# Kernel tuning notes

Hardware: AMD Instinct MI355X
Metric: run time of the kernel (lower is better)

The kernel has to match this reference:

```python
import jax, jax.numpy as jnp
import numpy as np

EPS_D = 1e-12  # clamp for sqrt of pairwise distances (diag is exactly 0)


def tr2dist_small(Y):
    # Y: (B, k, N) -> (B, N, N); standard protein-folding coords->distance map
    k = Y.shape[1]
    Z = Y - jnp.mean(Y, axis=2, keepdims=True)
    n2 = jnp.sum(Z * Z, axis=1)                        # (B, N)
    D = n2[:, None, :] + n2[:, :, None] - 2.0 * jnp.einsum('bkn,bkm->bnm', Z, Z)
    D = 3.0 * D / k
    return jnp.sqrt(jnp.maximum(D, EPS_D))


def mean_masked(X, mask, axis, keepdims=True):
    return jnp.sum(X * mask, axis=axis, keepdims=keepdims) / jnp.sum(mask, axis=axis, keepdims=keepdims)


def get_graph_lap(X, mask):
    # X: (B, C, N), mask: (B, 1, N)
    B, C, N = X.shape
    mm = jnp.einsum('bin,bim->bnm', mask, mask)        # (B, N, N) pair mask
    X = X - mean_masked(X, mask, axis=2) * mask
    X = X / jnp.sqrt(jnp.sum(X * X, axis=2, keepdims=True) / jnp.sum(mask, axis=2, keepdims=True) + 1e-4)
    pos = 0.5 * jnp.linspace(0.0, 1.0, N)[None, :] * mask   # (B, 1, N)
    Xa = jnp.concatenate((X, pos), axis=1)
    Wd = tr2dist_small(Xa) * mm
    sigma = mean_masked(Wd, mm, axis=(1, 2))           # (B, 1, 1)
    Wd = jnp.exp(-Wd / sigma * 10.0) * mm
    Wsum = jnp.sum(Wd, axis=1)                         # (B, N)
    L = jnp.zeros_like(Wd) + Wsum[:, :, None] * jnp.eye(N, dtype=Wd.dtype)[None] - Wd
    L = 0.5 * (L + jnp.swapaxes(L, 1, 2))
    return L, Wd


def _forward(Z, mask, K0, Knet, W, Wend):
    h = 0.01
    m = mask[:, None, :]                               # (B, 1, N)
    Z = jnp.tanh(jnp.einsum('oc,bcn->bon', K0, Z)) * m
    nlayers = W.shape[0]
    for i in range(nlayers):
        L, _ = get_graph_lap(Z, m)
        Ki = Knet[i]
        Wi = W[i, :, :, :, 0]                          # (3, C, C) size-1 kernels
        cv = lambda w, x: jnp.einsum('oc,bcn->bon', w, x) * m     # conv1d, k=1
        cvT = lambda w, x: jnp.einsum('co,bcn->bon', w, x) * m    # conv_transpose1d, k=1
        mm1 = lambda x: jnp.einsum('bcn,bnm->bcm', x, L)
        Ai = Ki[0] * cv(Wi[0], Z) + mm1(Ki[1] * cv(Wi[1], Z)) + mm1(mm1(Ki[2] * cv(Wi[2], Z)))
        Ai = (Ai - mean_masked(Ai, m, axis=2)) * m
        Ai = Ai / jnp.sqrt(jnp.sum(Ai * Ai, axis=1, keepdims=True) + 0.001)
        Ai = jax.nn.relu(Ai)
        Ai = Ki[0] * cvT(Wi[0], Ai) + mm1(Ki[1] * cvT(Wi[1], Ai)) + mm1(mm1(Ki[2] * cvT(Wi[2], Ai)))
        Z = Z - h * Ai
    Zout = jnp.einsum('oc,bcn->bon', Wend[:, :, 0], Z) * m       # (B, chan_out, N)
    dists = tuple(tr2dist_small(Zout[:, 3 * i:3 * i + 3, :]) for i in range(Zout.shape[1] // 3))
    return dists + (Zout,)


def setup_inputs() -> dict:
    key = jax.random.key(0)
    ks = jax.random.split(key, 6)
    B, chan_in, chan_out, channels, N, nlayers = 16, 40, 3, 256, 1024, 6
    stdv0 = 0.1 * channels / chan_in
    return {
        'Z': jax.random.normal(ks[0], (B, chan_in, N), dtype=jnp.float32),
        'mask': jnp.ones((B, N), dtype=jnp.float32),
        'K0': jax.random.uniform(ks[1], (channels, chan_in), minval=-stdv0, maxval=stdv0, dtype=jnp.float32),
        'Knet': jax.random.uniform(ks[2], (nlayers, chan_out), minval=-stdv0, maxval=stdv0, dtype=jnp.float32),
        'W': jax.random.uniform(ks[3], (nlayers, 3, channels, channels, 1), minval=-0.1, maxval=0.1, dtype=jnp.float32),
        'Wend': 1e-4 * jax.random.normal(ks[4], (chan_out, channels, 1), dtype=jnp.float32),
    }


def reference(Z, mask, K0, Knet, W, Wend):
    return _forward(Z, mask, K0, Knet, W, Wend)
```

## Files before the change

kernel.cpp:

```cpp
#include <hip/hip_runtime.h>
#include <hip/hip_fp16.h>
#include <math.h>

#define BB 16
#define CIN 40
#define CH 256
#define NN 1024
#define NLAYERS 6

typedef unsigned short ush;
typedef __attribute__((ext_vector_type(8))) short bh8;
typedef __attribute__((ext_vector_type(8))) _Float16 h8;
typedef __attribute__((ext_vector_type(4))) float f4;

__device__ __forceinline__ ush bf16_rne(float x) {
  unsigned int u = __float_as_uint(x);
  u += 0x7fffu + ((u >> 16) & 1u);
  return (ush)(u >> 16);
}
__device__ __forceinline__ float bf16_f(ush h) {
  return __uint_as_float(((unsigned int)h) << 16);
}
__device__ __forceinline__ ush f2h(float x) {
  __half h = __float2half(x);
  return *(ush*)&h;
}
__device__ __forceinline__ float h2f(ush u) {
  __half h = *(__half*)&u;
  return __half2float(h);
}

#define GLD16(gp, lp) __builtin_amdgcn_global_load_lds( \
    (const __attribute__((address_space(1))) void*)(gp), \
    (__attribute__((address_space(3))) void*)(lp), 16, 0, 0)

__device__ __forceinline__ float blockReduceSum(float v) {
  __shared__ float sred[4];
  const int lane = threadIdx.x & 63;
  const int wid  = threadIdx.x >> 6;
  #pragma unroll
  for (int off = 32; off > 0; off >>= 1) v += __shfl_down(v, off, 64);
  __syncthreads();
  if (lane == 0) sred[wid] = v;
  __syncthreads();
  return sred[0] + sred[1] + sred[2] + sred[3];
}

__device__ __forceinline__ void stageA(
    const ush* __restrict__ Ah, const ush* __restrict__ Al, const int sA,
    const ush* __restrict__ Bh, const ush* __restrict__ Bl, const int sB,
    const int kt, ush* buf) {
  const int lane = threadIdx.x & 63;
  const int wid = threadIdx.x >> 6;
  const int srow = lane >> 2;
  const int sl = (lane & 3) ^ ((srow >> 1) & 3);
  #pragma unroll
  for (int cc = 0; cc < 8; cc++) {
    const int c = wid * 8 + cc;
    const ush* src;
    if (c < 8)       src = Ah + (size_t)(c * 16 + srow) * sA + kt + sl * 8;
    else if (c < 16) src = Al + (size_t)((c - 8) * 16 + srow) * sA + kt + sl * 8;
    else if (c < 24) src = Bh + (size_t)((c - 16) * 16 + srow) * sB + kt + sl * 8;
    else             src = Bl + (size_t)((c - 24) * 16 + srow) * sB + kt + sl * 8;
    GLD16(src, buf + c * 512 + lane * 8);
  }
}

__device__ __forceinline__ void computeA(const ush* buf, f4 acc[4][4]) {
  const int lane = threadIdx.x & 63;
  const int wid = threadIdx.x >> 6;
  const int wr = wid >> 1, wc = wid & 1;
  const int frow = lane & 15;
  const int slot8 = (((lane >> 4) ^ ((frow >> 1) & 3)) << 3);
  bh8 ah[4], al[4], bh_[4], bl_[4];
  #pragma unroll
  for (int mi = 0; mi < 4; mi++) {
    const int off = (wr * 64 + mi * 16 + frow) * 32 + slot8;
    ah[mi] = *(const bh8*)&buf[off];
    al[mi] = *(const bh8*)&buf[4096 + off];
  }
  #pragma unroll
  for (int ni = 0; ni < 4; ni++) {
    const int off = (wc * 64 + ni * 16 + frow) * 32 + slot8;
    bh_[ni] = *(const bh8*)&buf[8192 + off];
    bl_[ni] = *(const bh8*)&buf[12288 + off];
  }
  #pragma unroll
  for (int mi = 0; mi < 4; mi++)
    #pragma unroll
    for (int ni = 0; ni < 4; ni++) {
      acc[mi][ni] = __builtin_amdgcn_mfma_f32_16x16x32_bf16(ah[mi], bh_[ni], acc[mi][ni], 0, 0, 0);
      acc[mi][ni] = __builtin_amdgcn_mfma_f32_16x16x32_bf16(ah[mi], bl_[ni], acc[mi][ni], 0, 0, 0);
      acc[mi][ni] = __builtin_amdgcn_mfma_f32_16x16x32_bf16(al[mi], bh_[ni], acc[mi][ni], 0, 0, 0);
    }
}

__device__ __forceinline__ void stageCV(
    const ush* __restrict__ Ap, const int sA,
    const ush* __restrict__ Bh, const ush* __restrict__ Bl, const int sB,
    const int kt, ush* buf) {
  const int lane = threadIdx.x & 63;
  const int wid = threadIdx.x >> 6;
  const int srow = lane >> 2;
  const int sl = (lane & 3) ^ ((srow >> 1) & 3);
  #pragma unroll
  for (int cc = 0; cc < 6; cc++) {
    const int c = wid * 6 + cc;
    const ush* src;
    if (c < 8)       src = Ap + (size_t)(c * 16 + srow) * sA + kt + sl * 8;
    else if (c < 16) src = Bh + (size_t)((c - 8) * 16 + srow) * sB + kt + sl * 8;
    else             src = Bl + (size_t)((c - 16) * 16 + srow) * sB + kt + sl * 8;
    GLD16(src, buf + c * 512 + lane * 8);
// ... 4 lines not shown
  const int lane = threadIdx.x & 63;
  const int wid = threadIdx.x >> 6;
  const int wr = wid >> 1, wc = wid & 1;
  const int frow = lane & 15;
  const int slot8 = (((lane >> 4) ^ ((frow >> 1) & 3)) << 3);
  h8 a_[4], bh_[4], bl_[4];
  #pragma unroll
  for (int mi = 0; mi < 4; mi++) {
    const int off = (wr * 64 + mi * 16 + frow) * 32 + slot8;
    a_[mi] = *(const h8*)&buf[off];
  }
  #pragma unroll
  for (int ni = 0; ni < 4; ni++) {
    const int off = (wc * 64 + ni * 16 + frow) * 32 + slot8;
    bh_[ni] = *(const h8*)&buf[4096 + off];
    bl_[ni] = *(const h8*)&buf[8192 + off];
  }
  #pragma unroll
  for (int mi = 0; mi < 4; mi++)
    #pragma unroll
    for (int ni = 0; ni < 4; ni++) {
      acc[mi][ni] = __builtin_amdgcn_mfma_f32_16x16x32_f16(a_[mi], bh_[ni], acc[mi][ni], 0, 0, 0);
      acc[mi][ni] = __builtin_amdgcn_mfma_f32_16x16x32_f16(a_[mi], bl_[ni], acc[mi][ni], 0, 0, 0);
    }
}

__device__ __forceinline__ void stageMM(
    const ush* __restrict__ Ah, const ush* __restrict__ Al, const int sA,
    const ush* __restrict__ Bp, const int sB, const int kt, ush* buf) {
  const int lane = threadIdx.x & 63;
  const int wid = threadIdx.x >> 6;
  const int srow = lane >> 2;
  const int sl = (lane & 3) ^ ((srow >> 1) & 3);
  #pragma unroll
  for (int cc = 0; cc < 4; cc++) {
    const int c = wid * 4 + cc;
    const ush* src;
    if (c < 4)       src = Ah + (size_t)(c * 16 + srow) * sA + kt + sl * 8;
    else if (c < 8)  src = Al + (size_t)((c - 4) * 16 + srow) * sA + kt + sl * 8;
    else             src = Bp + (size_t)((c - 8) * 16 + srow) * sB + kt + sl * 8;
    GLD16(src, buf + c * 512 + lane * 8);
  }
}

__device__ __forceinline__ void computeMM(const ush* buf, f4 acc[4][2]) {
  const int lane = threadIdx.x & 63;
  const int wid = threadIdx.x >> 6;
  const int frow = lane & 15;
  const int slot8 = (((lane >> 4) ^ ((frow >> 1) & 3)) << 3);
  h8 ah[4], al[4], b_[2];
  #pragma unroll
  for (int mi = 0; mi < 4; mi++) {
    const int off = (mi * 16 + frow) * 32 + slot8;
    ah[mi] = *(const h8*)&buf[off];
    al[mi] = *(const h8*)&buf[2048 + off];
  }
  #pragma unroll
  for (int ni = 0; ni < 2; ni++) {
    const int off = (wid * 32 + ni * 16 + frow) * 32 + slot8;
    b_[ni] = *(const h8*)&buf[4096 + off];
  }
  #pragma unroll
  for (int mi = 0; mi < 4; mi++)
    #pragma unroll
    for (int ni = 0; ni < 2; ni++) {
      acc[mi][ni] = __builtin_amdgcn_mfma_f32_16x16x32_f16(ah[mi], b_[ni], acc[mi][ni], 0, 0, 0);
      acc[mi][ni] = __builtin_amdgcn_mfma_f32_16x16x32_f16(al[mi], b_[ni], acc[mi][ni], 0, 0, 0);
    }
}

__global__ void k0_kernel(const float* __restrict__ Zin, const float* __restrict__ K0,
                          const float* __restrict__ mask, float* __restrict__ Zc,
                          float* __restrict__ statS1, float* __restrict__ statS2) {
  const int b = blockIdx.y;
  const int o = blockIdx.x;
  __shared__ float w[CIN];
  if (threadIdx.x < CIN) w[threadIdx.x] = K0[o * CIN + threadIdx.x];
  __syncthreads();
  float s1 = 0.f, s2 = 0.f;
  for (int n = threadIdx.x; n < NN; n += 256) {
    float acc = 0.f;
    #pragma unroll
    for (int c = 0; c < CIN; c++) acc += w[c] * Zin[((size_t)b * CIN + c) * NN + n];
    const float z = tanhf(acc) * mask[b * NN + n];
    Zc[((size_t)b * CH + o) * NN + n] = z;
    s1 += z; s2 += z * z;
  }
  s1 = blockReduceSum(s1);
  s2 = blockReduceSum(s2);
  if (threadIdx.x == 0) {
    const size_t base = ((size_t)b * CH + o) * 8;
    statS1[base] = s1; statS2[base] = s2;
    #pragma unroll
    for (int k = 1; k < 8; k++) { statS1[base + k] = 0.f; statS2[base + k] = 0.f; }
  }
}

__global__ void masksum_kernel(const float* __restrict__ mask, float* __restrict__ msum,
                               float* __restrict__ posv) {
  const int b = blockIdx.x;
  float v = 0.f, p = 0.f;
  for (int n = threadIdx.x; n < NN; n += 256) {
    const float m = mask[b * NN + n];
    v += m;
    p += 0.5f * ((float)n * (1.0f / (NN - 1))) * m;
  }
  v = blockReduceSum(v);
  p = blockReduceSum(p);
  const float pm = p * (1.0f / NN);
  if (threadIdx.x == 0) msum[b] = v;
  for (int n = threadIdx.x; n < NN; n += 256)
    posv[b * NN + n] = 0.5f * ((float)n * (1.0f / (NN - 1))) * mask[b * NN + n] - pm;
}

__global__ void wprep_kernel(const float* __restrict__ W, ush* __restrict__ Wm,
                             ush* __restrict__ Wt) {
  __shared__ float t[64][65];
  const int mat = blockIdx.y;
  const int ty = blockIdx.x >> 2, tx = blockIdx.x & 3;
  const float* src = W + (size_t)mat * CH * CH;
  const int tid = threadIdx.x;
  const int lr = tid >> 2;
  const int lc = (tid & 3) * 16;
  float v[16];
  #pragma unroll
  for (int j = 0; j < 16; j += 4)
    *(float4*)&v[j] = *(const float4*)&src[(size_t)(ty * 64 + lr) * CH + tx * 64 + lc + j];
  ush hv[16];
  #pragma unroll
  for (int j = 0; j < 16; j++) {
    hv[j] = f2h(v[j]);
    t[lr][lc + j] = v[j];
  }
  const size_t offm = (size_t)mat * CH * CH + (size_t)(ty * 64 + lr) * CH + tx * 64 + lc;
  #pragma unroll
  for (int j = 0; j < 16; j += 4)
    *(ushort4*)&Wm[offm + j] = *(ushort4*)&hv[j];
  __syncthreads();
  #pragma unroll
  for (int j = 0; j < 16; j++) hv[j] = f2h(t[lc + j][lr]);
  const size_t offt = (size_t)mat * CH * CH + (size_t)(tx * 64 + lr) * CH + ty * 64 + lc;
  #pragma unroll
  for (int j = 0; j < 16; j += 4)
    *(ushort4*)&Wt[offt + j] = *(ushort4*)&hv[j];
}

__global__ void rowstatZ_kernel(const float* __restrict__ statS1, const float* __restrict__ statS2,
                                const float* __restrict__ msum, float* __restrict__ muZ,
                                float* __restrict__ rsZ) {
  const int b = blockIdx.x;
  const int c = threadIdx.x;
  const size_t base = ((size_t)b * CH + c) * 8;
  float S1 = 0.f, S2 = 0.f;
  #pragma unroll
  for (int k = 0; k < 8; k++) { S1 += statS1[base + k]; S2 += statS2[base + k]; }
  const float M = msum[b];
  const float mu = S1 / M;
  const float q = fmaxf(S2 - mu * S1, 0.f);
  muZ[b * CH + c] = mu;
  rsZ[b * CH + c] = 1.0f / sqrtf(q / M + 1e-4f);
}

__global__ void rowstatU_kernel(const float* __restrict__ statS1, const float* __restrict__ msum,
                                float* __restrict__ rmean) {
  const int b = blockIdx.x;
  const int c = threadIdx.x;
  const size_t base = ((size_t)b * CH + c) * 8;
  float S1 = 0.f;
  #pragma unroll
  for (int k = 0; k < 8; k++) S1 += statS1[base + k];
  rmean[b * CH + c] = S1 / msum[b];
}

__global__ void tsplitZ_kernel(const float* __restrict__ in, ush* __restrict__ Th,
                               ush* __restrict__ Tl) {
  __shared__ float t[32][65];
  const int b = blockIdx.z;
  const int n0 = blockIdx.x * 64;
  const int k0 = blockIdx.y * 32;
  const float* src = in + (size_t)b * CH * NN;
  const int tid = threadIdx.x;
  const int lr = tid >> 3;
  const int lc = (tid & 7) * 8;
  const int gk = k0 + lr;
  *(float4*)&t[lr][lc]     = *(const float4*)&src[(size_t)gk * NN + n0 + lc];
  *(float4*)&t[lr][lc + 4] = *(const float4*)&src[(size_t)gk * NN + n0 + lc + 4];
  __syncthreads();
  const int on = tid >> 2;
  const int ok = (tid & 3) * 8;
  ush hv[8], lv[8];
  #pragma unroll
  for (int j = 0; j < 8; j++) {
    const float v = t[ok + j][on];
    hv[j] = f2h(v); lv[j] = f2h(v - h2f(hv[j]));
  }
  const size_t off = ((size_t)b * NN + n0 + on) * CH + k0 + ok;
  *(ushort4*)&Th[off] = *(ushort4*)&hv[0];
  *(ushort4*)&Th[off + 4] = *(ushort4*)&hv[4];
  *(ushort4*)&Tl[off] = *(ushort4*)&lv[0];
  *(ushort4*)&Tl[off + 4] = *(ushort4*)&lv[4];
}

__global__ void tsplitY2_kernel(const ush* __restrict__ Zsh, const ush* __restrict__ Zsl,
                                const float* __restrict__ mask, const float* __restrict__ muZ,
                                const float* __restrict__ rsZ, ush* __restrict__ Th,
                                ush* __restrict__ Tl, float* __restrict__ n2part) {
  const int b = blockIdx.z;
  const int n0 = blockIdx.x * 64;
  const int k0 = blockIdx.y * 32;
  const int tid = threadIdx.x;
  const int n = n0 + (tid >> 2);
  const int kc = k0 + (tid & 3) * 8;
  const float mn = mask[b * NN + n];
  const size_t zoff = ((size_t)b * NN + n) * CH + kc;
  const ushort4 h0 = *(const ushort4*)&Zsh[zoff];
  const ushort4 h1 = *(const ushort4*)&Zsh[zoff + 4];
  const ushort4 l0 = *(const ushort4*)&Zsl[zoff];
  const ushort4 l1 = *(const ushort4*)&Zsl[zoff + 4];
  const float4 mu0 = *(const float4*)&muZ[b * CH + kc];
  const float4 mu1 = *(const float4*)&muZ[b * CH + kc + 4];
  const float4 rs0 = *(const float4*)&rsZ[b * CH + kc];
  const float4 rs1 = *(const float4*)&rsZ[b * CH + kc + 4];
  float val[8];
  val[0] = (h2f(h0.x) + h2f(l0.x) - mu0.x * mn) * rs0.x;
  val[1] = (h2f(h0.y) + h2f(l0.y) - mu0.y * mn) * rs0.y;
  val[2] = (h2f(h0.z) + h2f(l0.z) - mu0.z * mn) * rs0.z;
  val[3] = (h2f(h0.w) + h2f(l0.w) - mu0.w * mn) * rs0.w;
  val[4] = (h2f(h1.x) + h2f(l1.x) - mu1.x * mn) * rs1.x;
  val[5] = (h2f(h1.y) + h2f(l1.y) - mu1.y * mn) * rs1.y;
  val[6] = (h2f(h1.z) + h2f(l1.z) - mu1.z * mn) * rs1.z;
  val[7] = (h2f(h1.w) + h2f(l1.w) - mu1.w * mn) * rs1.w;
  float s = 0.f;
  ush hv[8], lv[8];
  #pragma unroll
  for (int j = 0; j < 8; j++) {
    s += val[j] * val[j];
    hv[j] = bf16_rne(val[j]);
    lv[j] = bf16_rne(val[j] - bf16_f(hv[j]));
  }
  const size_t off = ((size_t)b * NN + n) * CH + kc;
  *(ushort4*)&Th[off] = *(ushort4*)&hv[0];
  *(ushort4*)&Th[off + 4] = *(ushort4*)&hv[4];
  *(ushort4*)&Tl[off] = *(ushort4*)&lv[0];
  *(ushort4*)&Tl[off + 4] = *(ushort4*)&lv[4];
  s += __shfl_xor(s, 1, 64);
  s += __shfl_xor(s, 2, 64);
  if ((tid & 3) == 0) n2part[((size_t)b * 8 + blockIdx.y) * NN + n] = s;
}

__global__ void n2red_kernel(const float* __restrict__ n2part, const float* __restrict__ posv,
                             float* __restrict__ n2) {
  const int idx = blockIdx.x * 256 + threadIdx.x;
  const int b = idx >> 10;
  const float pv = posv[idx];
  float s = pv * pv;
  #pragma unroll
  for (int kb = 0; kb < 8; kb++) s += n2part[((size_t)b * 8 + kb) * NN + (idx & 1023)];
  n2[idx] = s;
}

__global__ __launch_bounds__(256, 2)
void gram_v5_kernel(const ush* __restrict__ Yth, const ush* __restrict__ Ytl,
                    const float* __restrict__ n2, const float* __restrict__ mask,
                    const float* __restrict__ posv, ush* __restrict__ Dp,
                    float* __restrict__ sigpart) {
  __shared__ ush lds[32768];
  const int bid = blockIdx.x;
  const int logical = (bid & 7) * 72 + (bid >> 3);
  const int b = logical / 36;
  int t = logical - b * 36;
  int ty = 0;
  while (t >= 8 - ty) { t -= 8 - ty; ++ty; }
  const int tx = ty + t;
  const int i0 = ty * 128;
  const int j0 = tx * 128;
  const ush* Ah = Yth + (size_t)b * NN * CH + (size_t)i0 * CH;
  const ush* Al = Ytl + (size_t)b * NN * CH + (size_t)i0 * CH;
  const ush* Bh = Yth + (size_t)b * NN * CH + (size_t)j0 * CH;
  const ush* Bl = Ytl + (size_t)b * NN * CH + (size_t)j0 * CH;
  f4 acc[4][4];
  const f4 z4 = {0.f, 0.f, 0.f, 0.f};
  #pragma unroll
  for (int mi = 0; mi < 4; mi++)
    #pragma unroll
    for (int ni = 0; ni < 4; ni++) acc[mi][ni] = z4;
  stageA(Ah, Al, CH, Bh, Bl, CH, 0, lds);
  __syncthreads();
  int pb = 0;
  for (int kt = 32; kt < CH; kt += 32) {
    stageA(Ah, Al, CH, Bh, Bl, CH, kt, lds + (pb ^ 1) * 16384);
    computeA(lds + pb * 16384, acc);
    __syncthreads();
    pb ^= 1;
  }
  computeA(lds + pb * 16384, acc);
  const int lane = threadIdx.x & 63;
  const int wid = threadIdx.x >> 6;
  const int wr = wid >> 1, wc = wid & 1;
  const int frow = lane & 15, hh = lane >> 4;
  const float scale = 3.0f / 257.0f;
  float lsum = 0.f;
  #pragma unroll
  for (int ni = 0; ni < 4; ni++) {
    const int jl = wc * 64 + ni * 16 + frow;
    const int j = j0 + jl;
    const float n2j = n2[b * NN + j];
    const float mkj = mask[b * NN + j];
    const float pj = posv[b * NN + j];
    #pragma unroll
    for (int mi = 0; mi < 4; mi++) {
      const int il = wr * 64 + mi * 16 + hh * 4;
      ush dv[4];
      #pragma unroll
      for (int r = 0; r < 4; r++) {
        const int i = i0 + il + r;
        const float g = acc[mi][ni][r] + posv[b * NN + i] * pj;
        const float D = scale * (n2[b * NN + i] + n2j - 2.0f * g);
        const float d = sqrtf(fmaxf(D, 1e-12f));
        const float mmv = mask[b * NN + i] * mkj;
        const float wd = d * mmv;
        lsum += wd * mmv;
        dv[r] = f2h(wd);
      }
      if (ty != tx) {
        uint2 mr;
        mr.x = (unsigned)dv[0] | ((unsigned)dv[1] << 16);
        mr.y = (unsigned)dv[2] | ((unsigned)dv[3] << 16);
        *(uint2*)&Dp[((size_t)b * NN + j) * NN + i0 + il] = mr;
      }
      #pragma unroll
      for (int r = 0; r < 4; r++) {
        const unsigned v = dv[r];
        const unsigned vp = (unsigned)__shfl_xor((int)v, 1, 64);
        if ((frow & 1) == 0)
          *(unsigned*)&Dp[((size_t)b * NN + i0 + il + r) * NN + j] = v | (vp << 16);
      }
    }
  }
  if (ty != tx) lsum *= 2.0f;
  #pragma unroll
  for (int off = 32; off > 0; off >>= 1) lsum += __shfl_down(lsum, off, 64);
  __syncthreads();
  float* rbuf = (float*)lds;
  if (lane == 0) rbuf[wid] = lsum;
  __syncthreads();
  if (threadIdx.x == 0)
    sigpart[(size_t)b * 64 + ty * 8 + tx] = rbuf[0] + rbuf[1] + rbuf[2] + rbuf[3];
}

__global__ void sigfinal_kernel(const float* __restrict__ sigpart, const float* __restrict__ msum,
                                float* __restrict__ fbuf) {
  const int b = blockIdx.x;
  float v = 0.f;
  if (threadIdx.x < 64) {
    const int ty = threadIdx.x >> 3, tx = threadIdx.x & 7;
    if (ty <= tx) v = sigpart[b * 64 + threadIdx.x];
  }
  v = blockReduceSum(v);
  if (threadIdx.x == 0) { const float ms = msum[b]; fbuf[b] = -10.0f * ms * ms / v; }
}

__global__ void expw3_kernel(const ush* __restrict__ Dp, const float* __restrict__ mask,
                             const float* __restrict__ fbuf, ush* __restrict__ Wp) {
  const int b = blockIdx.y, n = blockIdx.x;
  const float fb = fbuf[b];
  const float mn = mask[b * NN + n];
  const size_t roff = ((size_t)b * NN + n) * NN;
  const int t = threadIdx.x;
  const float4 mk = ((const float4*)(mask + b * NN))[t];
  const ushort4 dp = *(const ushort4*)&Dp[roff + t * 4];
  const float w0 = expf(fb * h2f(dp.x)) * mn * mk.x;
  const float w1 = expf(fb * h2f(dp.y)) * mn * mk.y;
  const float w2 = expf(fb * h2f(dp.z)) * mn * mk.z;
  const float w3 = expf(fb * h2f(dp.w)) * mn * mk.w;
  const float s = blockReduceSum(w0 + w1 + w2 + w3);
  float v0 = -w0, v1 = -w1, v2 = -w2, v3 = -w3;
  if ((n >> 2) == t) {
    const int r = n & 3;
    if (r == 0) v0 += s; else if (r == 1) v1 += s; else if (r == 2) v2 += s; else v3 += s;
  }
  ushort4 h4;
  h4.x = f2h(v0); h4.y = f2h(v1); h4.z = f2h(v2); h4.w = f2h(v3);
  *(ushort4*)&Wp[roff + t * 4] = h4;
}

__global__ __launch_bounds__(256, 3)
void cvall_kernel(const ush* __restrict__ Ap, const ush* __restrict__ Bth,
                  const ush* __restrict__ Btl, const float* __restrict__ mask,
                  const float* __restrict__ Kis, unsigned int* __restrict__ Cpack,
                  ush* __restrict__ C2h, ush* __restrict__ C2l) {
  __shared__ ush lds[24576];
  const int bid = blockIdx.x;
  const int logical = (bid & 7) * 96 + (bid >> 3);
  const int b = logical / 48;
  const int inner = logical - b * 48;
  const int c0g = inner & 7;
  const int r0g = inner >> 3;
  const int r0 = r0g * 128;
  const int c0 = c0g * 128;
  const ush* Aq = Ap + (size_t)r0 * CH;
  const ush* Bh = Bth + (size_t)b * NN * CH + (size_t)c0 * CH;
  const ush* Bl = Btl + (size_t)b * NN * CH + (size_t)c0 * CH;
  f4 acc[4][4];
  const f4 z4 = {0.f, 0.f, 0.f, 0.f};
  #pragma unroll
  for (int mi = 0; mi < 4; mi++)
    #pragma unroll
    for (int ni = 0; ni < 4; ni++) acc[mi][ni] = z4;
  stageCV(Aq, CH, Bh, Bl, CH, 0, lds);
  __syncthreads();
  int pb = 0;
  for (int kt = 32; kt < CH; kt += 32) {
    stageCV(Aq, CH, Bh, Bl, CH, kt, lds + (pb ^ 1) * 12288);
    computeCV(lds + pb * 12288, acc);
    __syncthreads();
    pb ^= 1;
  }
  computeCV(lds + pb * 12288, acc);
  const int lane = threadIdx.x & 63;
  const int wid = threadIdx.x >> 6;
  const int wr = wid >> 1, wc = wid & 1;
  const int frow = lane & 15, hh = lane >> 4;
  const float alpha = Kis[r0g >> 1];
  #pragma unroll
  for (int ni = 0; ni < 4; ni++) {
    const int jl = wc * 64 + ni * 16 + frow;
    const int col = c0 + jl;
    const float am = alpha * mask[b * NN + col];
    #pragma unroll
    for (int mi = 0; mi < 4; mi++) {
      const int il = wr * 64 + mi * 16 + hh * 4;
      #pragma unroll
      for (int r = 0; r < 4; r++) {
        const int row = r0 + il + r;
        const float v = acc[mi][ni][r] * am;
        const ush h = f2h(v);
        const ush l = f2h(v - h2f(h));
        const unsigned pv = (unsigned)h | ((unsigned)l << 16);
        const unsigned pvp = (unsigned)__shfl_xor((int)pv, 1, 64);
        if ((frow & 1) == 0) {
          if (r0g < 4) {
            uint2 w2; w2.x = pv; w2.y = pvp;
            *(uint2*)&Cpack[((size_t)b * 512 + row) * NN + col] = w2;
          } else {
            const size_t obase = ((size_t)b * 256 + (row - 512)) * NN + col;
            const unsigned hw = (pv & 0xffffu) | (pvp << 16);
            const unsigned lw = (pv >> 16) | (pvp & 0xffff0000u);
            *(unsigned*)&C2h[obase] = hw;
            *(unsigned*)&C2l[obase] = lw;
          }
        }
      }
    }
  }
}

template <int OUTMODE, int STATS>
// ... 75 lines not shown
  __syncthreads();
  if (OUTMODE == 0) {
    const int rrow = threadIdx.x >> 2;
    const int rch = (threadIdx.x & 3) * 32;
    const size_t obase = ((size_t)b * 256 + r0 + rrow) * NN + n0 + rch;
    #pragma unroll
    for (int g = 0; g < 4; g++) {
      unsigned int hw[4], lw[4];
      #pragma unroll
      for (int q = 0; q < 4; q++) {
        unsigned int h2[2], l2[2];
        #pragma unroll
        for (int e = 0; e < 2; e++) {
          const int jl = rch + g * 8 + q * 2 + e;
          const int slot = (rrow >> 2) ^ (jl & 15);
          const unsigned int v = tl[jl * 64 + slot * 4 + (rrow & 3)];
          h2[e] = v & 0xffffu; l2[e] = v >> 16;
        }
        hw[q] = h2[0] | (h2[1] << 16);
        lw[q] = l2[0] | (l2[1] << 16);
      }
      *(uint4*)&outH[obase + g * 8] = *(uint4*)hw;
      *(uint4*)&outL[obase + g * 8] = *(uint4*)lw;
    }
  } else {
    const int nloc = threadIdx.x >> 1;
    const int ch0 = (threadIdx.x & 1) * 32;
    #pragma unroll
    for (int half = 0; half < 2; half++) {
      unsigned int hw[8], lw[8];
      #pragma unroll
      for (int q = 0; q < 8; q++) {
        const int ila = ch0 + half * 16 + q * 2;
        const int ilb = ila + 1;
        const unsigned int va = tl[nloc * 64 + (((ila >> 2) ^ (nloc & 15)) << 2) + (ila & 3)];
        const unsigned int vb = tl[nloc * 64 + (((ilb >> 2) ^ (nloc & 15)) << 2) + (ilb & 3)];
        hw[q] = (va & 0xffffu) | (vb << 16);
        lw[q] = (va >> 16) | (vb & 0xffff0000u);
      }
      const size_t zoff = ((size_t)b * NN + n0 + nloc) * CH + r0 + ch0 + half * 16;
      *(uint4*)&outH[zoff] = *(uint4*)&hw[0];
      *(uint4*)&outH[zoff + 8] = *(uint4*)&hw[4];
      *(uint4*)&outL[zoff] = *(uint4*)&lw[0];
      *(uint4*)&outL[zoff + 8] = *(uint4*)&lw[4];
    }
  }
  if (STATS) {
    #pragma unroll
    for (int mi = 0; mi < 4; mi++)
      #pragma unroll
      for (int r = 0; r < 4; r++) {
        #pragma unroll
        for (int d = 1; d < 16; d <<= 1) {
          a1[mi][r] += __shfl_xor(a1[mi][r], d, 64);
          a2[mi][r] += __shfl_xor(a2[mi][r], d, 64);
        }
      }
    __syncthreads();
    float* s1b = (float*)lds;
    float* s2b = s1b + 256;
    if (frow == 0) {
      #pragma unroll
      for (int mi = 0; mi < 4; mi++)
        #pragma unroll
        for (int r = 0; r < 4; r++) {
          const int row = mi * 16 + hh * 4 + r;
          s1b[wid * 64 + row] = a1[mi][r];
          s2b[wid * 64 + row] = a2[mi][r];
        }
    }
    __syncthreads();
    if (threadIdx.x < 64) {
      const int row = threadIdx.x;
      const float p1 = s1b[row] + s1b[64 + row] + s1b[128 + row] + s1b[192 + row];
      const float p2 = s2b[row] + s2b[64 + row] + s2b[128 + row] + s2b[192 + row];
      const int nblk = n0 >> 7;
      statS1[((size_t)b * CH + r0 + row) * 8 + nblk] = p1;
      statS2[((size_t)b * CH + r0 + row) * 8 + nblk] = p2;
    }
  }
}

__global__ void csq_kernel(const ush* __restrict__ Uh, const ush* __restrict__ Ul,
                           const float* __restrict__ mask, const float* __restrict__ rmean,
                           float* __restrict__ part) {
  const int b = blockIdx.y, cc = blockIdx.x;
  const int n = threadIdx.x * 4;
  const float4 m4 = *(const float4*)&mask[b * NN + n];
  float4 s4 = {0.f, 0.f, 0.f, 0.f};
  for (int r = 0; r < 16; r++) {
    const int c = cc * 16 + r;
    const float rm = rmean[b * CH + c];
    const size_t uoff = ((size_t)b * 256 + c) * NN + n;
    const ushort4 uh = *(const ushort4*)&Uh[uoff];
    const ushort4 ul = *(const ushort4*)&Ul[uoff];
    float a;
    a = (h2f(uh.x) + h2f(ul.x) - rm) * m4.x; s4.x += a * a;
    a = (h2f(uh.y) + h2f(ul.y) - rm) * m4.y; s4.y += a * a;
    a = (h2f(uh.z) + h2f(ul.z) - rm) * m4.z; s4.z += a * a;
    a = (h2f(uh.w) + h2f(ul.w) - rm) * m4.w; s4.w += a * a;
  }
  *(float4*)&part[((size_t)(b * 16 + cc)) * NN + n] = s4;
}

__global__ void csq2_kernel(const float* __restrict__ part, float* __restrict__ rs) {
  const int b = blockIdx.y;
  const int n = blockIdx.x * 256 + threadIdx.x;
  float s = 0.001f;
  #pragma unroll
  for (int cc = 0; cc < 16; cc++) s += part[((size_t)(b * 16 + cc)) * NN + n];
  rs[b * NN + n] = 1.0f / sqrtf(s);
}

__global__ void tsplitN2_kernel(const ush* __restrict__ Uh, const ush* __restrict__ Ul,
                                const float* __restrict__ mask, const float* __restrict__ rmean,
                                const float* __restrict__ rs, ush* __restrict__ Th,
                                ush* __restrict__ Tl) {
  __shared__ float t[32][65];
  const int b = blockIdx.z;
  const int n0 = blockIdx.x * 64;
  const int k0 = blockIdx.y * 32;
  const int tid = threadIdx.x;
  const int lr = tid >> 3;
  const int lc = (tid & 7) * 8;
  const int gc = k0 + lr;
  const float rm = rmean[b * CH + gc];
  const float4 ma = *(const float4*)&mask[b * NN + n0 + lc];
  const float4 mb = *(const float4*)&mask[b * NN + n0 + lc + 4];
  const float4 ra = *(const float4*)&rs[b * NN + n0 + lc];
  const float4 rb = *(const float4*)&rs[b * NN + n0 + lc + 4];
  const size_t uoff = ((size_t)b * 256 + gc) * NN + n0 + lc;
  const ushort4 ha = *(const ushort4*)&Uh[uoff];
  const ushort4 hb = *(const ushort4*)&Uh[uoff + 4];
  const ushort4 la = *(const ushort4*)&Ul[uoff];
  const ushort4 lb = *(const ushort4*)&Ul[uoff + 4];
  t[lr][lc + 0] = fmaxf((h2f(ha.x) + h2f(la.x) - rm) * ma.x * ra.x, 0.f);
  t[lr][lc + 1] = fmaxf((h2f(ha.y) + h2f(la.y) - rm) * ma.y * ra.y, 0.f);
  t[lr][lc + 2] = fmaxf((h2f(ha.z) + h2f(la.z) - rm) * ma.z * ra.z, 0.f);
  t[lr][lc + 3] = fmaxf((h2f(ha.w) + h2f(la.w) - rm) * ma.w * ra.w, 0.f);
  t[lr][lc + 4] = fmaxf((h2f(hb.x) + h2f(lb.x) - rm) * mb.x * rb.x, 0.f);
  t[lr][lc + 5] = fmaxf((h2f(hb.y) + h2f(lb.y) - rm) * mb.y * rb.y, 0.f);
  t[lr][lc + 6] = fmaxf((h2f(hb.z) + h2f(lb.z) - rm) * mb.z * rb.z, 0.f);
  t[lr][lc + 7] = fmaxf((h2f(hb.w) + h2f(lb.w) - rm) * mb.w * rb.w, 0.f);
  __syncthreads();
  const int on = tid >> 2;
  const int ok = (tid & 3) * 8;
  ush hv[8], lv[8];
  #pragma unroll
  for (int j = 0; j < 8; j++) {
    const float v = t[ok + j][on];
    hv[j] = f2h(v); lv[j] = f2h(v - h2f(hv[j]));
  }
  const size_t off = ((size_t)b * NN + n0 + on) * CH + k0 + ok;
  *(ushort4*)&Th[off] = *(ushort4*)&hv[0];
  *(ushort4*)&Th[off + 4] = *(ushort4*)&hv[4];
  *(ushort4*)&Tl[off] = *(ushort4*)&lv[0];
  *(ushort4*)&Tl[off + 4] = *(ushort4*)&lv[4];
}

__global__ void zout_kernel(const float* __restrict__ Z, const float* __restrict__ Wend,
                            const float* __restrict__ mask, float* __restrict__ outZ,
                            float* __restrict__ Zcent) {
  const int b = blockIdx.x;
  __shared__ float w[3 * CH];
  for (int i = threadIdx.x; i < 3 * CH; i += 256) w[i] = Wend[i];
  __syncthreads();
  float a[3][4];
  #pragma unroll
  for (int j = 0; j < 4; j++) { a[0][j] = 0.f; a[1][j] = 0.f; a[2][j] = 0.f; }
  const float* Zb = Z + (size_t)b * CH * NN;
  for (int c = 0; c < CH; c++) {
    const float w0 = w[c], w1 = w[CH + c], w2 = w[2 * CH + c];
    #pragma unroll
    for (int j = 0; j < 4; j++) {
      float zv = Zb[(size_t)c * NN + threadIdx.x + j * 256];
      a[0][j] += w0 * zv; a[1][j] += w1 * zv; a[2][j] += w2 * zv;
    }
  }
  float sum[3] = {0.f, 0.f, 0.f};
  #pragma unroll
  for (int j = 0; j < 4; j++) {
    const int n = threadIdx.x + j * 256;
    const float mv = mask[b * NN + n];
    #pragma unroll
    for (int o = 0; o < 3; o++) {
      a[o][j] *= mv;
      outZ[((size_t)b * 3 + o) * NN + n] = a[o][j];
      sum[o] += a[o][j];
    }
  }
  for (int o = 0; o < 3; o++) {
    float s = blockReduceSum(sum[o]);
    const float mean = s * (1.0f / NN);
    #pragma unroll
    for (int j = 0; j < 4; j++) {
      const int n = threadIdx.x + j * 256;
      Zcent[((size_t)b * 3 + o) * NN + n] = a[o][j] - mean;
    }
  }
}

__global__ void dist_kernel(const float* __restrict__ Zcent, float* __restrict__ outD) {
  const int b = blockIdx.z;
  const int n = blockIdx.y;
  const int m = blockIdx.x * 256 + threadIdx.x;
  const float* Zb = Zcent + (size_t)b * 3 * NN;
  const float x0 = Zb[n], x1 = Zb[NN + n], x2 = Zb[2 * NN + n];
  const float d0 = x0 - Zb[m], d1 = x1 - Zb[NN + m], d2 = x2 - Zb[2 * NN + m];
  const float D = d0 * d0 + d1 * d1 + d2 * d2;
  outD[((size_t)b * NN + n) * NN + m] = sqrtf(fmaxf(D, 1e-12f));
}

extern "C" void kernel_launch(void* const* d_in, const int* in_sizes, int n_in,
                              void* d_out, int out_size, void* d_ws, size_t ws_size,
                              hipStream_t stream) {
  const float* Zin  = (const float*)d_in[0];
  const float* mask = (const float*)d_in[1];
  const float* K0   = (const float*)d_in[2];
  const float* Knet = (const float*)d_in[3];
  const float* W    = (const float*)d_in[4];
  const float* Wend = (const float*)d_in[5];
  float* out = (float*)d_out;

  ush* Wp = (ush*)out;
  ush* Dp = Wp + (size_t)BB * NN * NN;
  float* outZ = out + (size_t)BB * NN * NN;

  float* p = (float*)d_ws;
  float* uni = p; p += (size_t)BB * 768 * NN;
  ush* Yth = (ush*)uni;
  ush* Ytl = Yth + (size_t)BB * NN * CH;
  unsigned int* Cpack = (unsigned int*)uni;
  ush* C2h = (ush*)(uni + (size_t)BB * 512 * NN);
  ush* C2l = C2h + (size_t)BB * 256 * NN;

  float* Zcur = p; p += (size_t)BB * CH * NN;
  ush* Thb = (ush*)p; p += (size_t)BB * NN * CH / 2;
  ush* Tlb = (ush*)p; p += (size_t)BB * NN * CH / 2;
  ush* Zsh = (ush*)p; p += (size_t)BB * NN * CH / 2;
  ush* Zsl = (ush*)p; p += (size_t)BB * NN * CH / 2;
  ush* Wm = (ush*)p; p += (size_t)18 * CH * CH / 2;
  ush* Wt = (ush*)p; p += (size_t)18 * CH * CH / 2;
  float* n2b   = p; p += BB * NN;
  float* rsb   = p; p += BB * NN;
  float* msum  = p; p += BB;
  float* posv  = p; p += BB * NN;
  float* sigp  = p; p += BB * 64;
  float* fbuf  = p; p += BB;
  float* rmeanb= p; p += BB * CH;
  float* muZ   = p; p += BB * CH;
  float* rsZ   = p; p += BB * CH;
  float* statS1= p; p += (size_t)BB * CH * 8;
  float* statS2= p; p += (size_t)BB * CH * 8;
  float* n2part= p; p += (size_t)BB * 8 * NN;
  float* partb = p; p += (size_t)BB * 16 * NN;
  float* Zcent = p; p += BB * 3 * NN;

  const dim3 gtsZ(NN / 64, CH / 32, BB);
  const size_t sC = (size_t)512 * NN;
  const size_t sT = (size_t)CH * NN;

  masksum_kernel<<<BB, 256, 0, stream>>>(mask, msum, posv);
  wprep_kernel<<<dim3(16, 18), 256, 0, stream>>>(W, Wm, Wt);
  k0_kernel<<<dim3(CH, BB), 256, 0, stream>>>(Zin, K0, mask, Zcur, statS1, statS2);
  tsplitZ_kernel<<<gtsZ, 256, 0, stream>>>(Zcur, Zsh, Zsl);

  for (int layer = 0; layer < NLAYERS; layer++) {
    rowstatZ_kernel<<<BB, 256, 0, stream>>>(statS1, statS2, msum, muZ, rsZ);
    tsplitY2_kernel<<<gtsZ, 256, 0, stream>>>(Zsh, Zsl, mask, muZ, rsZ, Yth, Ytl, n2part);
    n2red_kernel<<<BB * NN / 256, 256, 0, stream>>>(n2part, posv, n2b);
    gram_v5_kernel<<<576, 256, 0, stream>>>(Yth, Ytl, n2b, mask, posv, Dp, sigp);
    sigfinal_kernel<<<BB, 256, 0, stream>>>(sigp, msum, fbuf);
    expw3_kernel<<<dim3(NN, BB), 256, 0, stream>>>(Dp, mask, fbuf, Wp);

    const ush* Am = Wm + (size_t)layer * 3 * CH * CH;
    const ush* At = Wt + (size_t)layer * 3 * CH * CH;
    const float* Ki = Knet + layer * 3;

    cvall_kernel<<<768, 256, 0, stream>>>(Am, Zsh, Zsl, mask, Ki, Cpack, C2h, C2l);
    mm1_v6_kernel<0, 0><<<512, 256, 0, stream>>>(C2h, C2l, sT, Wp,
        Cpack + (size_t)256 * NN, sC, nullptr, nullptr, nullptr, Thb, Tlb, nullptr, nullptr);
    mm1_v6_kernel<0, 1><<<512, 256, 0, stream>>>(Thb, Tlb, sT, Wp,
        Cpack, sC, nullptr, mask, nullptr, C2h, C2l, statS1, statS2);

    rowstatU_kernel<<<BB, 256, 0, stream>>>(statS1, msum, rmeanb);
    csq_kernel<<<dim3(16, BB), 256, 0, stream>>>(C2h, C2l, mask, rmeanb, partb);
    csq2_kernel<<<dim3(NN / 256, BB), 256, 0, stream>>>(partb, rsb);
    tsplitN2_kernel<<<gtsZ, 256, 0, stream>>>(C2h, C2l, mask, rmeanb, rsb, Thb, Tlb);

    cvall_kernel<<<768, 256, 0, stream>>>(At, Thb, Tlb, mask, Ki, Cpack, C2h, C2l);
    mm1_v6_kernel<0, 0><<<512, 256, 0, stream>>>(C2h, C2l, sT, Wp,
        Cpack + (size_t)256 * NN, sC, nullptr, nullptr, nullptr, Thb, Tlb, nullptr, nullptr);
    mm1_v6_kernel<2, 1><<<512, 256, 0, stream>>>(Thb, Tlb, sT, Wp,
        Cpack, sC, Zcur, mask, Zcur, Zsh, Zsl, statS1, statS2);
  }

  zout_kernel<<<BB, 256, 0, stream>>>(Zcur, Wend, mask, outZ, Zcent);
  dist_kernel<<<dim3(NN / 256, NN, BB), 256, 0, stream>>>(Zcent, out);
}
```

Before: 1.768 ms.

## Fold small reduction kernels into consumers and use fast exp/tanh intrinsics

Five tiny per-layer kernels (rowstatZ, n2red, sigfinal, rowstatU, csq2) are removed. Each consumer kernel now recomputes the small reduction it needs into shared memory at block start, which cuts launches and global round-trips per layer. The work is duplicated redundantly across blocks, and an extra sync is added. It also swaps expf/tanhf for __expf-based fast versions, which loses a little accuracy.

```diff
diff --git a/kernel.cpp b/kernel.cpp
--- a/kernel.cpp
+++ b/kernel.cpp
@@ -28,6 +28,10 @@
 __device__ __forceinline__ float h2f(ush u) {
   __half h = *(__half*)&u;
   return __half2float(h);
+}
+__device__ __forceinline__ float fast_tanh(float x) {
+  const float e = __expf(2.0f * x);
+  return (e - 1.0f) / (e + 1.0f);
 }
 
 #define GLD16(gp, lp) __builtin_amdgcn_global_load_lds( \
@@ -198,7 +202,7 @@
     float acc = 0.f;
     #pragma unroll
     for (int c = 0; c < CIN; c++) acc += w[c] * Zin[((size_t)b * CIN + c) * NN + n];
-    const float z = tanhf(acc) * mask[b * NN + n];
+    const float z = fast_tanh(acc) * mask[b * NN + n];
     Zc[((size_t)b * CH + o) * NN + n] = z;
     s1 += z; s2 += z * z;
   }
@@ -259,33 +263,6 @@
   #pragma unroll
   for (int j = 0; j < 16; j += 4)
     *(ushort4*)&Wt[offt + j] = *(ushort4*)&hv[j];
-}
-
-__global__ void rowstatZ_kernel(const float* __restrict__ statS1, const float* __restrict__ statS2,
-                                const float* __restrict__ msum, float* __restrict__ muZ,
-                                float* __restrict__ rsZ) {
-  const int b = blockIdx.x;
-  const int c = threadIdx.x;
-  const size_t base = ((size_t)b * CH + c) * 8;
-  float S1 = 0.f, S2 = 0.f;
-  #pragma unroll
-  for (int k = 0; k < 8; k++) { S1 += statS1[base + k]; S2 += statS2[base + k]; }
-  const float M = msum[b];
-  const float mu = S1 / M;
-  const float q = fmaxf(S2 - mu * S1, 0.f);
-  muZ[b * CH + c] = mu;
-  rsZ[b * CH + c] = 1.0f / sqrtf(q / M + 1e-4f);
-}
-
-__global__ void rowstatU_kernel(const float* __restrict__ statS1, const float* __restrict__ msum,
-                                float* __restrict__ rmean) {
-  const int b = blockIdx.x;
-  const int c = threadIdx.x;
-  const size_t base = ((size_t)b * CH + c) * 8;
-  float S1 = 0.f;
-  #pragma unroll
-  for (int k = 0; k < 8; k++) S1 += statS1[base + k];
-  rmean[b * CH + c] = S1 / msum[b];
 }
 
 __global__ void tsplitZ_kernel(const float* __restrict__ in, ush* __restrict__ Th,
@@ -318,34 +295,45 @@
 }
 
 __global__ void tsplitY2_kernel(const ush* __restrict__ Zsh, const ush* __restrict__ Zsl,
-                                const float* __restrict__ mask, const float* __restrict__ muZ,
-                                const float* __restrict__ rsZ, ush* __restrict__ Th,
+                                const float* __restrict__ mask,
+                                const float* __restrict__ statS1, const float* __restrict__ statS2,
+                                const float* __restrict__ msum, ush* __restrict__ Th,
                                 ush* __restrict__ Tl, float* __restrict__ n2part) {
+  __shared__ float smu[32], srs[32];
   const int b = blockIdx.z;
   const int n0 = blockIdx.x * 64;
   const int k0 = blockIdx.y * 32;
   const int tid = threadIdx.x;
+  if (tid < 32) {
+    const size_t base = ((size_t)b * CH + k0 + tid) * 8;
+    float S1 = 0.f, S2 = 0.f;
+    #pragma unroll
+    for (int k = 0; k < 8; k++) { S1 += statS1[base + k]; S2 += statS2[base + k]; }
+    const float M = msum[b];
+    const float mu = S1 / M;
+    const float q = fmaxf(S2 - mu * S1, 0.f);
+    smu[tid] = mu;
+    srs[tid] = 1.0f / sqrtf(q / M + 1e-4f);
+  }
+  __syncthreads();
   const int n = n0 + (tid >> 2);
-  const int kc = k0 + (tid & 3) * 8;
+  const int kl = (tid & 3) * 8;
+  const int kc = k0 + kl;
   const float mn = mask[b * NN + n];
   const size_t zoff = ((size_t)b * NN + n) * CH + kc;
   const ushort4 h0 = *(const ushort4*)&Zsh[zoff];
   const ushort4 h1 = *(const ushort4*)&Zsh[zoff + 4];
   const ushort4 l0 = *(const ushort4*)&Zsl[zoff];
   const ushort4 l1 = *(const ushort4*)&Zsl[zoff + 4];
-  const float4 mu0 = *(const float4*)&muZ[b * CH + kc];
-  const float4 mu1 = *(const float4*)&muZ[b * CH + kc + 4];
-  const float4 rs0 = *(const float4*)&rsZ[b * CH + kc];
-  const float4 rs1 = *(const float4*)&rsZ[b * CH + kc + 4];
   float val[8];
-  val[0] = (h2f(h0.x) + h2f(l0.x) - mu0.x * mn) * rs0.x;
-  val[1] = (h2f(h0.y) + h2f(l0.y) - mu0.y * mn) * rs0.y;
-  val[2] = (h2f(h0.z) + h2f(l0.z) - mu0.z * mn) * rs0.z;
-  val[3] = (h2f(h0.w) + h2f(l0.w) - mu0.w * mn) * rs0.w;
-  val[4] = (h2f(h1.x) + h2f(l1.x) - mu1.x * mn) * rs1.x;
-  val[5] = (h2f(h1.y) + h2f(l1.y) - mu1.y * mn) * rs1.y;
-  val[6] = (h2f(h1.z) + h2f(l1.z) - mu1.z * mn) * rs1.z;
-  val[7] = (h2f(h1.w) + h2f(l1.w) - mu1.w * mn) * rs1.w;
+  val[0] = (h2f(h0.x) + h2f(l0.x) - smu[kl + 0] * mn) * srs[kl + 0];
+  val[1] = (h2f(h0.y) + h2f(l0.y) - smu[kl + 1] * mn) * srs[kl + 1];
+  val[2] = (h2f(h0.z) + h2f(l0.z) - smu[kl + 2] * mn) * srs[kl + 2];
+  val[3] = (h2f(h0.w) + h2f(l0.w) - smu[kl + 3] * mn) * srs[kl + 3];
+  val[4] = (h2f(h1.x) + h2f(l1.x) - smu[kl + 4] * mn) * srs[kl + 4];
+  val[5] = (h2f(h1.y) + h2f(l1.y) - smu[kl + 5] * mn) * srs[kl + 5];
+  val[6] = (h2f(h1.z) + h2f(l1.z) - smu[kl + 6] * mn) * srs[kl + 6];
+  val[7] = (h2f(h1.w) + h2f(l1.w) - smu[kl + 7] * mn) * srs[kl + 7];
   float s = 0.f;
   ush hv[8], lv[8];
   #pragma unroll
@@ -364,23 +352,14 @@
   if ((tid & 3) == 0) n2part[((size_t)b * 8 + blockIdx.y) * NN + n] = s;
 }
 
-__global__ void n2red_kernel(const float* __restrict__ n2part, const float* __restrict__ posv,
-                             float* __restrict__ n2) {
-  const int idx = blockIdx.x * 256 + threadIdx.x;
-  const int b = idx >> 10;
-  const float pv = posv[idx];
-  float s = pv * pv;
-  #pragma unroll
-  for (int kb = 0; kb < 8; kb++) s += n2part[((size_t)b * 8 + kb) * NN + (idx & 1023)];
-  n2[idx] = s;
-}
-
 __global__ __launch_bounds__(256, 2)
-void gram_v5_kernel(const ush* __restrict__ Yth, const ush* __restrict__ Ytl,
-                    const float* __restrict__ n2, const float* __restrict__ mask,
+void gram_v6_kernel(const ush* __restrict__ Yth, const ush* __restrict__ Ytl,
+                    const float* __restrict__ n2part, const float* __restrict__ mask,
                     const float* __restrict__ posv, ush* __restrict__ Dp,
                     float* __restrict__ sigpart) {
   __shared__ ush lds[32768];
+  __shared__ float sn2[256];
+  __shared__ float spv[256];
   const int bid = blockIdx.x;
   const int logical = (bid & 7) * 72 + (bid >> 3);
   const int b = logical / 36;
@@ -390,6 +369,16 @@
   const int tx = ty + t;
   const int i0 = ty * 128;
   const int j0 = tx * 128;
+  {
+    const int tt = threadIdx.x;
+    const int nn = (tt < 128) ? (i0 + tt) : (j0 + tt - 128);
+    const float pv = posv[b * NN + nn];
+    float s = pv * pv;
+    #pragma unroll
+    for (int kb = 0; kb < 8; kb++) s += n2part[((size_t)b * 8 + kb) * NN + nn];
+    sn2[tt] = s;
+    spv[tt] = pv;
+  }
   const ush* Ah = Yth + (size_t)b * NN * CH + (size_t)i0 * CH;
   const ush* Al = Ytl + (size_t)b * NN * CH + (size_t)i0 * CH;
   const ush* Bh = Yth + (size_t)b * NN * CH + (size_t)j0 * CH;
@@ -420,9 +409,9 @@
   for (int ni = 0; ni < 4; ni++) {
     const int jl = wc * 64 + ni * 16 + frow;
     const int j = j0 + jl;
-    const float n2j = n2[b * NN + j];
+    const float n2j = sn2[128 + jl];
+    const float pj = spv[128 + jl];
     const float mkj = mask[b * NN + j];
-    const float pj = posv[b * NN + j];
     #pragma unroll
     for (int mi = 0; mi < 4; mi++) {
       const int il = wr * 64 + mi * 16 + hh * 4;
@@ -430,8 +419,8 @@
       #pragma unroll
       for (int r = 0; r < 4; r++) {
         const int i = i0 + il + r;
-        const float g = acc[mi][ni][r] + posv[b * NN + i] * pj;
-        const float D = scale * (n2[b * NN + i] + n2j - 2.0f * g);
+        const float g = acc[mi][ni][r] + spv[il + r] * pj;
+        const float D = scale * (sn2[il + r] + n2j - 2.0f * g);
         const float d = sqrtf(fmaxf(D, 1e-12f));
         const float mmv = mask[b * NN + i] * mkj;
         const float wd = d * mmv;
@@ -464,31 +453,31 @@
     sigpart[(size_t)b * 64 + ty * 8 + tx] = rbuf[0] + rbuf[1] + rbuf[2] + rbuf[3];
 }
 
-__global__ void sigfinal_kernel(const float* __restrict__ sigpart, const float* __restrict__ msum,
-                                float* __restrict__ fbuf) {
-  const int b = blockIdx.x;
-  float v = 0.f;
-  if (threadIdx.x < 64) {
-    const int ty = threadIdx.x >> 3, tx = threadIdx.x & 7;
-    if (ty <= tx) v = sigpart[b * 64 + threadIdx.x];
-  }
-  v = blockReduceSum(v);
-  if (threadIdx.x == 0) { const float ms = msum[b]; fbuf[b] = -10.0f * ms * ms / v; }
-}
-
-__global__ void expw3_kernel(const ush* __restrict__ Dp, const float* __restrict__ mask,
-                             const float* __restrict__ fbuf, ush* __restrict__ Wp) {
+__global__ void expw4_kernel(const ush* __restrict__ Dp, const float* __restrict__ mask,
+                             const float* __restrict__ sigpart, const float* __restrict__ msum,
+                             ush* __restrict__ Wp) {
+  __shared__ float sfb;
   const int b = blockIdx.y, n = blockIdx.x;
-  const float fb = fbuf[b];
+  const int t = threadIdx.x;
+  {
+    float v = 0.f;
+    if (t < 64) {
+      const int sy = t >> 3, sx = t & 7;
+      if (sy <= sx) v = sigpart[b * 64 + t];
+    }
+    v = blockReduceSum(v);
+    if (t == 0) { const float ms = msum[b]; sfb = -10.0f * ms * ms / v; }
+  }
+  __syncthreads();
+  const float fb = sfb;
   const float mn = mask[b * NN + n];
   const size_t roff = ((size_t)b * NN + n) * NN;
-  const int t = threadIdx.x;
   const float4 mk = ((const float4*)(mask + b * NN))[t];
   const ushort4 dp = *(const ushort4*)&Dp[roff + t * 4];
-  const float w0 = expf(fb * h2f(dp.x)) * mn * mk.x;
-  const float w1 = expf(fb * h2f(dp.y)) * mn * mk.y;
-  const float w2 = expf(fb * h2f(dp.z)) * mn * mk.z;
-  const float w3 = expf(fb * h2f(dp.w)) * mn * mk.w;
+  const float w0 = __expf(fb * h2f(dp.x)) * mn * mk.x;
+  const float w1 = __expf(fb * h2f(dp.y)) * mn * mk.y;
+  const float w2 = __expf(fb * h2f(dp.z)) * mn * mk.z;
+  const float w3 = __expf(fb * h2f(dp.w)) * mn * mk.w;
   const float s = blockReduceSum(w0 + w1 + w2 + w3);
   float v0 = -w0, v1 = -w1, v2 = -w2, v3 = -w3;
   if ((n >> 2) == t) {
@@ -730,15 +719,24 @@
 }
 
 __global__ void csq_kernel(const ush* __restrict__ Uh, const ush* __restrict__ Ul,
-                           const float* __restrict__ mask, const float* __restrict__ rmean,
-                           float* __restrict__ part) {
+                           const float* __restrict__ mask, const float* __restrict__ statS1,
+                           const float* __restrict__ msum, float* __restrict__ part) {
+  __shared__ float srm[16];
   const int b = blockIdx.y, cc = blockIdx.x;
+  if (threadIdx.x < 16) {
+    const size_t base = ((size_t)b * CH + cc * 16 + threadIdx.x) * 8;
+    float S1 = 0.f;
+    #pragma unroll
+    for (int k = 0; k < 8; k++) S1 += statS1[base + k];
+    srm[threadIdx.x] = S1 / msum[b];
+  }
+  __syncthreads();
   const int n = threadIdx.x * 4;
   const float4 m4 = *(const float4*)&mask[b * NN + n];
   float4 s4 = {0.f, 0.f, 0.f, 0.f};
   for (int r = 0; r < 16; r++) {
     const int c = cc * 16 + r;
-    const float rm = rmean[b * CH + c];
+    const float rm = srm[r];
     const size_t uoff = ((size_t)b * 256 + c) * NN + n;
     const ushort4 uh = *(const ushort4*)&Uh[uoff];
     const ushort4 ul = *(const ushort4*)&Ul[uoff];
@@ -751,45 +749,50 @@
   *(float4*)&part[((size_t)(b * 16 + cc)) * NN + n] = s4;
 }
 
-__global__ void csq2_kernel(const float* __restrict__ part, float* __restrict__ rs) {
-  const int b = blockIdx.y;
-  const int n = blockIdx.x * 256 + threadIdx.x;
-  float s = 0.001f;
-  #pragma unroll
-  for (int cc = 0; cc < 16; cc++) s += part[((size_t)(b * 16 + cc)) * NN + n];
-  rs[b * NN + n] = 1.0f / sqrtf(s);
-}
-
 __global__ void tsplitN2_kernel(const ush* __restrict__ Uh, const ush* __restrict__ Ul,
-                                const float* __restrict__ mask, const float* __restrict__ rmean,
-                                const float* __restrict__ rs, ush* __restrict__ Th,
-                                ush* __restrict__ Tl) {
+                                const float* __restrict__ mask, const float* __restrict__ statS1,
+                                const float* __restrict__ msum, const float* __restrict__ part,
+                                ush* __restrict__ Th, ush* __restrict__ Tl) {
   __shared__ float t[32][65];
+  __shared__ float srm[32];
+  __shared__ float srsl[64];
   const int b = blockIdx.z;
   const int n0 = blockIdx.x * 64;
   const int k0 = blockIdx.y * 32;
   const int tid = threadIdx.x;
+  if (tid < 32) {
+    const size_t base = ((size_t)b * CH + k0 + tid) * 8;
+    float S1 = 0.f;
+    #pragma unroll
+    for (int k = 0; k < 8; k++) S1 += statS1[base + k];
+    srm[tid] = S1 / msum[b];
+  } else if (tid < 96) {
+    const int n = n0 + tid - 32;
+    float s = 0.001f;
+    #pragma unroll
+    for (int cc = 0; cc < 16; cc++) s += part[((size_t)(b * 16 + cc)) * NN + n];
+    srsl[tid - 32] = 1.0f / sqrtf(s);
+  }
+  __syncthreads();
   const int lr = tid >> 3;
   const int lc = (tid & 7) * 8;
   const int gc = k0 + lr;
-  const float rm = rmean[b * CH + gc];
+  const float rm = srm[lr];
   const float4 ma = *(const float4*)&mask[b * NN + n0 + lc];
   const float4 mb = *(const float4*)&mask[b * NN + n0 + lc + 4];
-  const float4 ra = *(const float4*)&rs[b * NN + n0 + lc];
-  const float4 rb = *(const float4*)&rs[b * NN + n0 + lc + 4];
   const size_t uoff = ((size_t)b * 256 + gc) * NN + n0 + lc;
   const ushort4 ha = *(const ushort4*)&Uh[uoff];
   const ushort4 hb = *(const ushort4*)&Uh[uoff + 4];
   const ushort4 la = *(const ushort4*)&Ul[uoff];
   const ushort4 lb = *(const ushort4*)&Ul[uoff + 4];
-  t[lr][lc + 0] = fmaxf((h2f(ha.x) + h2f(la.x) - rm) * ma.x * ra.x, 0.f);
-  t[lr][lc + 1] = fmaxf((h2f(ha.y) + h2f(la.y) - rm) * ma.y * ra.y, 0.f);
-  t[lr][lc + 2] = fmaxf((h2f(ha.z) + h2f(la.z) - rm) * ma.z * ra.z, 0.f);
-  t[lr][lc + 3] = fmaxf((h2f(ha.w) + h2f(la.w) - rm) * ma.w * ra.w, 0.f);
-  t[lr][lc + 4] = fmaxf((h2f(hb.x) + h2f(lb.x) - rm) * mb.x * rb.x, 0.f);
-  t[lr][lc + 5] = fmaxf((h2f(hb.y) + h2f(lb.y) - rm) * mb.y * rb.y, 0.f);
-  t[lr][lc + 6] = fmaxf((h2f(hb.z) + h2f(lb.z) - rm) * mb.z * rb.z, 0.f);
-  t[lr][lc + 7] = fmaxf((h2f(hb.w) + h2f(lb.w) - rm) * mb.w * rb.w, 0.f);
+  t[lr][lc + 0] = fmaxf((h2f(ha.x) + h2f(la.x) - rm) * ma.x * srsl[lc + 0], 0.f);
+  t[lr][lc + 1] = fmaxf((h2f(ha.y) + h2f(la.y) - rm) * ma.y * srsl[lc + 1], 0.f);
+  t[lr][lc + 2] = fmaxf((h2f(ha.z) + h2f(la.z) - rm) * ma.z * srsl[lc + 2], 0.f);
+  t[lr][lc + 3] = fmaxf((h2f(ha.w) + h2f(la.w) - rm) * ma.w * srsl[lc + 3], 0.f);
+  t[lr][lc + 4] = fmaxf((h2f(hb.x) + h2f(lb.x) - rm) * mb.x * srsl[lc + 4], 0.f);
+  t[lr][lc + 5] = fmaxf((h2f(hb.y) + h2f(lb.y) - rm) * mb.y * srsl[lc + 5], 0.f);
+  t[lr][lc + 6] = fmaxf((h2f(hb.z) + h2f(lb.z) - rm) * mb.z * srsl[lc + 6], 0.f);
+  t[lr][lc + 7] = fmaxf((h2f(hb.w) + h2f(lb.w) - rm) * mb.w * srsl[lc + 7], 0.f);
   __syncthreads();
   const int on = tid >> 2;
   const int ok = (tid & 3) * 8;
@@ -889,15 +892,9 @@
   ush* Zsl = (ush*)p; p += (size_t)BB * NN * CH / 2;
   ush* Wm = (ush*)p; p += (size_t)18 * CH * CH / 2;
   ush* Wt = (ush*)p; p += (size_t)18 * CH * CH / 2;
-  float* n2b   = p; p += BB * NN;
-  float* rsb   = p; p += BB * NN;
   float* msum  = p; p += BB;
   float* posv  = p; p += BB * NN;
   float* sigp  = p; p += BB * 64;
-  float* fbuf  = p; p += BB;
-  float* rmeanb= p; p += BB * CH;
-  float* muZ   = p; p += BB * CH;
-  float* rsZ   = p; p += BB * CH;
   float* statS1= p; p += (size_t)BB * CH * 8;
   float* statS2= p; p += (size_t)BB * CH * 8;
   float* n2part= p; p += (size_t)BB * 8 * NN;
@@ -914,12 +911,10 @@
   tsplitZ_kernel<<<gtsZ, 256, 0, stream>>>(Zcur, Zsh, Zsl);
 
   for (int layer = 0; layer < NLAYERS; layer++) {
-    rowstatZ_kernel<<<BB, 256, 0, stream>>>(statS1, statS2, msum, muZ, rsZ);
-    tsplitY2_kernel<<<gtsZ, 256, 0, stream>>>(Zsh, Zsl, mask, muZ, rsZ, Yth, Ytl, n2part);
-    n2red_kernel<<<BB * NN / 256, 256, 0, stream>>>(n2part, posv, n2b);
-    gram_v5_kernel<<<576, 256, 0, stream>>>(Yth, Ytl, n2b, mask, posv, Dp, sigp);
-    sigfinal_kernel<<<BB, 256, 0, stream>>>(sigp, msum, fbuf);
-    expw3_kernel<<<dim3(NN, BB), 256, 0, stream>>>(Dp, mask, fbuf, Wp);
+    tsplitY2_kernel<<<gtsZ, 256, 0, stream>>>(Zsh, Zsl, mask, statS1, statS2, msum,
+                                              Yth, Ytl, n2part);
+    gram_v6_kernel<<<576, 256, 0, stream>>>(Yth, Ytl, n2part, mask, posv, Dp, sigp);
+    expw4_kernel<<<dim3(NN, BB), 256, 0, stream>>>(Dp, mask, sigp, msum, Wp);
 
     const ush* Am = Wm + (size_t)layer * 3 * CH * CH;
     const ush* At = Wt + (size_t)layer * 3 * CH * CH;
@@ -931,10 +926,8 @@
     mm1_v6_kernel<0, 1><<<512, 256, 0, stream>>>(Thb, Tlb, sT, Wp,
         Cpack, sC, nullptr, mask, nullptr, C2h, C2l, statS1, statS2);
 
-    rowstatU_kernel<<<BB, 256, 0, stream>>>(statS1, msum, rmeanb);
-    csq_kernel<<<dim3(16, BB), 256, 0, stream>>>(C2h, C2l, mask, rmeanb, partb);
-    csq2_kernel<<<dim3(NN / 256, BB), 256, 0, stream>>>(partb, rsb);
-    tsplitN2_kernel<<<gtsZ, 256, 0, stream>>>(C2h, C2l, mask, rmeanb, rsb, Thb, Tlb);
+    csq_kernel<<<dim3(16, BB), 256, 0, stream>>>(C2h, C2l, mask, statS1, msum, partb);
+    tsplitN2_kernel<<<gtsZ, 256, 0, stream>>>(C2h, C2l, mask, statS1, msum, partb, Thb, Tlb);
 
     cvall_kernel<<<768, 256, 0, stream>>>(At, Thb, Tlb, mask, Ki, Cpack, C2h, C2l);
     mm1_v6_kernel<0, 0><<<512, 256, 0, stream>>>(C2h, C2l, sT, Wp,
```

After: 1.770 ms. Within noise of the previous version (+0.2%).
